# Kernel optimization log

Measured on AMD Instinct MI355X. Metric: run time of the kernel, lower is better.

## Reference

```python
import jax, jax.numpy as jnp
import numpy as np

B, T = 2, 512
E, NH, HD, V, P, L, KER, BLOCK = 768, 12, 64, 256, 4, 4, 16, 512
SCALE = HD ** -0.5


def _ln(x, g, b, eps=1e-5):
    m = jnp.mean(x, -1, keepdims=True)
    v = jnp.mean((x - m) ** 2, -1, keepdims=True)
    return (x - m) * jax.lax.rsqrt(v + eps) * g + b


def _rope_tables(n):
    inv = 1.0 / (10000.0 ** (jnp.arange(0, HD, 2, dtype=jnp.float32) / HD))
    f = jnp.arange(n, dtype=jnp.float32)[:, None] * inv[None, :]
    return jnp.cos(f), jnp.sin(f)


def _rope(x, cos, sin):
    # rotate over last two dims (positions, HD); split-half RoPE as in source
    h = x.shape[-1] // 2
    x1, x2 = x[..., :h], x[..., h:]
    return jnp.concatenate([x1 * cos - x2 * sin, x1 * sin + x2 * cos], axis=-1)


def _patch_attn(x, qkv_w, S):
    # x: [B,T,E]; sliding-window patch attention, step=1
    Bb, Tt, _ = x.shape
    q, k, v = jnp.split(x @ qkv_w, 3, axis=-1)
    heads = lambda t: t.reshape(Bb, Tt, NH, HD).transpose(0, 2, 1, 3)  # [B,NH,T,HD]
    q, k, v = heads(q), heads(k), heads(v)
    cos, sin = _rope_tables(Tt)
    q = _rope(q, cos, sin)
    k = _rope(k, cos, sin)
    # prefix: full causal attention over first S tokens
    sc = jnp.einsum('bnqh,bnkh->bnqk', q[:, :, :S], k[:, :, :S]) * SCALE
    mask = jnp.tril(jnp.ones((S, S), dtype=bool))
    sc = jnp.where(mask, sc, jnp.float32(-jnp.inf))
    out = jnp.einsum('bnqk,bnkh->bnqh', jax.nn.softmax(sc, axis=-1), v[:, :, :S])
    if Tt > S:
        # query t (t>=S) attends keys [t-S+1, t] (mask_sliding is all-ones for step=1)
        idx = jnp.arange(Tt - S)[:, None] + 1 + jnp.arange(S)[None, :]  # [T-S,S]
        kw = k[:, :, idx]  # [B,NH,T-S,S,HD]
        vw = v[:, :, idx]
        qs = q[:, :, S:]   # [B,NH,T-S,HD]
        sw = jnp.einsum('bnth,bntsh->bnts', qs, kw) * SCALE
        ow = jnp.einsum('bnts,bntsh->bnth', jax.nn.softmax(sw, axis=-1), vw)
        out = jnp.concatenate([out, ow], axis=2)
    return out.transpose(0, 2, 1, 3).reshape(Bb, Tt, NH * HD)


def _sa_block(x, ln0g, ln0b, ln1g, ln1b, qkv_w, proj_w, proj_b, w1, b1, w2, b2):
    # x: [B,T,P,V]; full (unmasked) attention over the P prediction slots
    Bb, Tt, Pp, _ = x.shape
    h = _ln(x, ln0g, ln0b)
    q, k, v = jnp.split(h @ qkv_w, 3, axis=-1)
    heads = lambda t: t.reshape(Bb, Tt, Pp, NH, HD).transpose(0, 1, 3, 2, 4)  # [B,T,NH,P,HD]
    q, k, v = heads(q), heads(k), heads(v)
    cos, sin = _rope_tables(Pp)
    q = _rope(q, cos, sin)
    k = _rope(k, cos, sin)
    sc = jnp.einsum('btnph,btnqh->btnpq', q, k) * SCALE
    o = jnp.einsum('btnpq,btnqh->btnph', jax.nn.softmax(sc, axis=-1), v)
    o = o.transpose(0, 1, 3, 2, 4).reshape(Bb, Tt, Pp, NH * HD)
    x = x + (o @ proj_w + proj_b)
    h2 = _ln(x, ln1g, ln1b)
    ff = jax.nn.gelu(h2 @ w1 + b1, approximate=False) @ w2 + b2
    return x + ff


def _forward(tokens, emb, blk_ln0_g, blk_ln0_b, blk_ln1_g, blk_ln1_b, blk_qkv_w,
             blk_ff_w1, blk_ff_b1, blk_ff_w2, blk_ff_b2, fin_ln_g, fin_ln_b,
             head_w, head_b, sa_ln0_g, sa_ln0_b, sa_ln1_g, sa_ln1_b, sa_qkv_w,
             sa_proj_w, sa_proj_b, sa_ff_w1, sa_ff_b1, sa_ff_w2, sa_ff_b2):
    x0 = emb[tokens]  # [B,T,E]
    x = x0
    for i in range(L):
        S = min(KER * 2 ** i, BLOCK)
        h = _ln(x, blk_ln0_g[i], blk_ln0_b[i])
        x = x + _patch_attn(h, blk_qkv_w[i], S)
        h2 = _ln(x, blk_ln1_g[i], blk_ln1_b[i])
        x = x + (jax.nn.gelu(h2 @ blk_ff_w1[i] + blk_ff_b1[i], approximate=False)
                 @ blk_ff_w2[i] + blk_ff_b2[i])
    x = x0 + x  # Golu: x = token_embedding(x); x = x + blocks(x)
    x = _ln(x, fin_ln_g, fin_ln_b)
    logits = (x @ head_w + head_b).reshape(B, T, P, V)
    logits = _sa_block(logits, sa_ln0_g, sa_ln0_b, sa_ln1_g, sa_ln1_b, sa_qkv_w,
                       sa_proj_w, sa_proj_b, sa_ff_w1, sa_ff_b1, sa_ff_w2, sa_ff_b2)
    return logits[:, :, 0, :]  # [B,T,V] (y is None path)


def setup_inputs() -> dict:
    key = jax.random.key(0)
    ks = jax.random.split(key, 12)
    w = lambda k, sh: jax.random.normal(k, sh, dtype=jnp.float32) * 0.02
    return {
        'tokens': jax.random.randint(ks[0], (B, T), 0, V),
        'emb': w(ks[1], (V, E)),
        'blk_ln0_g': jnp.ones((L, E), jnp.float32),
        'blk_ln0_b': jnp.zeros((L, E), jnp.float32),
        'blk_ln1_g': jnp.ones((L, E), jnp.float32),
        'blk_ln1_b': jnp.zeros((L, E), jnp.float32),
        'blk_qkv_w': w(ks[2], (L, E, 3 * E)),
        'blk_ff_w1': w(ks[3], (L, E, 4 * E)),
        'blk_ff_b1': jnp.zeros((L, 4 * E), jnp.float32),
        'blk_ff_w2': w(ks[4], (L, 4 * E, E)),
        'blk_ff_b2': jnp.zeros((L, E), jnp.float32),
        'fin_ln_g': jnp.ones((E,), jnp.float32),
        'fin_ln_b': jnp.zeros((E,), jnp.float32),
        'head_w': w(ks[5], (E, V * P)),
        'head_b': jnp.zeros((V * P,), jnp.float32),
        'sa_ln0_g': jnp.ones((V,), jnp.float32),
        'sa_ln0_b': jnp.zeros((V,), jnp.float32),
        'sa_ln1_g': jnp.ones((V,), jnp.float32),
        'sa_ln1_b': jnp.zeros((V,), jnp.float32),
        'sa_qkv_w': w(ks[6], (V, 3 * E)),
        'sa_proj_w': w(ks[7], (E, V)),
        'sa_proj_b': jnp.zeros((V,), jnp.float32),
        'sa_ff_w1': w(ks[8], (V, 4 * V)),
        'sa_ff_b1': jnp.zeros((4 * V,), jnp.float32),
        'sa_ff_w2': w(ks[9], (4 * V, V)),
        'sa_ff_b2': jnp.zeros((V,), jnp.float32),
    }


def reference(tokens, emb, blk_ln0_g, blk_ln0_b, blk_ln1_g, blk_ln1_b, blk_qkv_w,
              blk_ff_w1, blk_ff_b1, blk_ff_w2, blk_ff_b2, fin_ln_g, fin_ln_b,
              head_w, head_b, sa_ln0_g, sa_ln0_b, sa_ln1_g, sa_ln1_b, sa_qkv_w,
              sa_proj_w, sa_proj_b, sa_ff_w1, sa_ff_b1, sa_ff_w2, sa_ff_b2):
    return _forward(tokens, emb, blk_ln0_g, blk_ln0_b, blk_ln1_g, blk_ln1_b,
                    blk_qkv_w, blk_ff_w1, blk_ff_b1, blk_ff_w2, blk_ff_b2,
                    fin_ln_g, fin_ln_b, head_w, head_b, sa_ln0_g, sa_ln0_b,
                    sa_ln1_g, sa_ln1_b, sa_qkv_w, sa_proj_w, sa_proj_b,
                    sa_ff_w1, sa_ff_b1, sa_ff_w2, sa_ff_b2)
```

## Files before the change

### kernel.cpp

```cpp
#include <hip/hip_runtime.h>
#include <hip/hip_bf16.h>
#include <cstdint>
#include <cstddef>

#define BB    2
#define TSEQ  512
#define EDIM  768
#define NHEAD 12
#define HDIM  64
#define VDIM  256
#define PDIM  4
#define NROW  (BB*TSEQ)
#define NROW2 (BB*TSEQ*PDIM)

typedef __attribute__((ext_vector_type(8))) short short8;
typedef __attribute__((ext_vector_type(4))) float floatx4;

__device__ __forceinline__ float gelu_f(float v){
    return 0.5f * v * (1.0f + erff(v * 0.70710678118654752f));
}
__device__ __forceinline__ float b2f(short s){
    unsigned u = ((unsigned)(unsigned short)s) << 16;
    float f; __builtin_memcpy(&f, &u, 4); return f;
}
__device__ __forceinline__ short f2bs(float v){
    __hip_bfloat16 h = __float2bfloat16(v);
    short s; __builtin_memcpy(&s, &h, 2); return s;
}
__device__ __forceinline__ void gload16(const void* g, void* l){
    __builtin_amdgcn_global_load_lds((const __attribute__((address_space(1))) void*)g,
                                     (__attribute__((address_space(3))) void*)l, 16, 0, 0);
}

struct WD2 { const float* in; __hip_bfloat16* out; int K; int N; int nt; };
struct WDs { WD2 d[17]; };

__global__ __launch_bounds__(256) void wconv_all(WDs a)
{
    int id = blockIdx.x;
    int i = 0;
    while(i < 16 && id >= a.d[i].nt){ id -= a.d[i].nt; i++; }
    WD2 w = a.d[i];
    const int tx = w.N / 64;
    const int n0 = (id % tx) * 64, k0 = (id / tx) * 64;
    __shared__ float t[64][65];
    const int cg = (threadIdx.x & 15) * 4;
    const int rr = threadIdx.x >> 4;
    #pragma unroll
    for(int it = 0; it < 4; it++){
        int r = rr + it*16;
        float4 v = *(const float4*)(w.in + (size_t)(k0 + r) * w.N + n0 + cg);
        t[r][cg+0] = v.x; t[r][cg+1] = v.y; t[r][cg+2] = v.z; t[r][cg+3] = v.w;
    }
    __syncthreads();
    #pragma unroll
    for(int it = 0; it < 4; it++){
        int n = rr + it*16;
        short4 o;
        o.x = f2bs(t[cg+0][n]); o.y = f2bs(t[cg+1][n]);
        o.z = f2bs(t[cg+2][n]); o.w = f2bs(t[cg+3][n]);
        *(short4*)((short*)w.out + (size_t)(n0 + n) * w.K + k0 + cg) = o;
    }
}

template<int ACT, int RESID, int OUTBF16, int ROPESA>
__global__ __launch_bounds__(256) void gemm128(
    const short* __restrict__ A, const short* __restrict__ Bt,
    const float* __restrict__ bias, const float* __restrict__ resid,
    void* __restrict__ Cout, const float* __restrict__ rc, const float* __restrict__ rs,
    int M, int N, int K)
{
    alignas(16) __shared__ short As[128*32];
    alignas(16) __shared__ short Bs[128*32];
    const int tid  = threadIdx.x;
    const int lane = tid & 63;
    const int wave = tid >> 6;
    const int bm = blockIdx.y * 128, bn = blockIdx.x * 128;
    const int wm = (wave >> 1) * 64, wn = (wave & 1) * 64;
    const int quad = lane >> 4, l16 = lane & 15;

    floatx4 acc[4][4];
    #pragma unroll
    for(int i = 0; i < 4; i++)
        #pragma unroll
        for(int j = 0; j < 4; j++)
            acc[i][j] = floatx4{0.f, 0.f, 0.f, 0.f};

    const int r  = tid >> 2;
    const int c8 = (tid & 3) * 8;
    const int ldsoff = (tid & 192) * 16;

    for(int k0 = 0; k0 < K; k0 += 32){
        gload16(A  + (size_t)(bm + r     ) * K + k0 + c8, (char*)As + ldsoff);
        gload16(A  + (size_t)(bm + r + 64) * K + k0 + c8, (char*)As + 4096 + ldsoff);
        gload16(Bt + (size_t)(bn + r     ) * K + k0 + c8, (char*)Bs + ldsoff);
        gload16(Bt + (size_t)(bn + r + 64) * K + k0 + c8, (char*)Bs + 4096 + ldsoff);
        __syncthreads();
        short8 af[4], bfr[4];
        #pragma unroll
        for(int i = 0; i < 4; i++){
            af[i]  = *(const short8*)&As[(wm + i*16 + l16)*32 + quad*8];
            bfr[i] = *(const short8*)&Bs[(wn + i*16 + l16)*32 + quad*8];
        }
        #pragma unroll
        for(int i = 0; i < 4; i++)
            #pragma unroll
            for(int j = 0; j < 4; j++)
                acc[i][j] = __builtin_amdgcn_mfma_f32_16x16x32_bf16(af[i], bfr[j], acc[i][j], 0, 0, 0);
        __syncthreads();
    }

    float* Cf = (float*)Cout;
    __hip_bfloat16* Cb = (__hip_bfloat16*)Cout;

    if(ROPESA){
        const int hb = bn + wn;
        const int region = hb / 768;
        #pragma unroll
        for(int i = 0; i < 4; i++){
            #pragma unroll
            for(int rr = 0; rr < 4; rr++){
                int row = bm + wm + i*16 + quad*4 + rr;
                float a0 = acc[i][0][rr], a1 = acc[i][1][rr];
                float a2 = acc[i][2][rr], a3 = acc[i][3][rr];
                size_t rowb = (size_t)row * N + hb;
                if(region == 2){
                    Cb[rowb + l16]      = __float2bfloat16(a0);
                    Cb[rowb + 16 + l16] = __float2bfloat16(a1);
                    Cb[rowb + 32 + l16] = __float2bfloat16(a2);
                    Cb[rowb + 48 + l16] = __float2bfloat16(a3);
                }else{
                    int p = row & 3;
                    float c0 = rc[p*32 + l16],      s0 = rs[p*32 + l16];
                    float c1 = rc[p*32 + 16 + l16], s1 = rs[p*32 + 16 + l16];
                    Cb[rowb + l16]      = __float2bfloat16(a0*c0 - a2*s0);
                    Cb[rowb + 16 + l16] = __float2bfloat16(a1*c1 - a3*s1);
                    Cb[rowb + 32 + l16] = __float2bfloat16(a0*s0 + a2*c0);
                    Cb[rowb + 48 + l16] = __float2bfloat16(a1*s1 + a3*c1);
                }
            }
        }
        return;
    }

    #pragma unroll
    for(int i = 0; i < 4; i++){
        int row0 = bm + wm + i*16 + quad*4;
        #pragma unroll
        for(int j = 0; j < 4; j++){
            int col = bn + wn + j*16 + l16;
            float bv = bias ? bias[col] : 0.f;
            #pragma unroll
            for(int rr = 0; rr < 4; rr++){
                float v = acc[i][j][rr] + bv;
                if(ACT) v = gelu_f(v);
                if(RESID) v += resid[(size_t)(row0 + rr) * N + col];
                if(OUTBF16) Cb[(size_t)(row0 + rr) * N + col] = __float2bfloat16(v);
                else        Cf[(size_t)(row0 + rr) * N + col] = v;
            }
        }
    }
}

template<int EPI>
__global__ __launch_bounds__(256) void gemm64x128(
    const short* __restrict__ A, const short* __restrict__ Bt,
    const float* __restrict__ bias, __hip_bfloat16* __restrict__ Cout,
    __hip_bfloat16* __restrict__ qrb, __hip_bfloat16* __restrict__ krb,
    __hip_bfloat16* __restrict__ vvb,
    const float* __restrict__ rc, const float* __restrict__ rs,
    int M, int N, int K)
{
    alignas(16) __shared__ short As[64*32];
    alignas(16) __shared__ short Bs[128*32];
    const int tid  = threadIdx.x;
    const int lane = tid & 63;
    const int wave = tid >> 6;
    const int bm = blockIdx.y * 64, bn = blockIdx.x * 128;
    const int wm = (wave >> 1) * 32, wn = (wave & 1) * 64;
    const int quad = lane >> 4, l16 = lane & 15;

    floatx4 acc[2][4];
    #pragma unroll
    for(int i = 0; i < 2; i++)
        #pragma unroll
        for(int j = 0; j < 4; j++)
            acc[i][j] = floatx4{0.f, 0.f, 0.f, 0.f};

    const int r  = tid >> 2;
    const int c8 = (tid & 3) * 8;
    const int ldsoff = (tid & 192) * 16;

    for(int k0 = 0; k0 < K; k0 += 32){
        gload16(A  + (size_t)(bm + r     ) * K + k0 + c8, (char*)As + ldsoff);
        gload16(Bt + (size_t)(bn + r     ) * K + k0 + c8, (char*)Bs + ldsoff);
        gload16(Bt + (size_t)(bn + r + 64) * K + k0 + c8, (char*)Bs + 4096 + ldsoff);
        __syncthreads();
        short8 af[2], bfr[4];
        #pragma unroll
        for(int i = 0; i < 2; i++)
            af[i]  = *(const short8*)&As[(wm + i*16 + l16)*32 + quad*8];
        #pragma unroll
        for(int j = 0; j < 4; j++)
            bfr[j] = *(const short8*)&Bs[(wn + j*16 + l16)*32 + quad*8];
        #pragma unroll
        for(int i = 0; i < 2; i++)
            #pragma unroll
            for(int j = 0; j < 4; j++)
                acc[i][j] = __builtin_amdgcn_mfma_f32_16x16x32_bf16(af[i], bfr[j], acc[i][j], 0, 0, 0);
        __syncthreads();
    }

    if(EPI == 2){
        const int hb = bn + wn;
        const int region = hb / 768;
        const int h = (hb % 768) >> 6;
        #pragma unroll
        for(int i = 0; i < 2; i++){
            #pragma unroll
            for(int rr = 0; rr < 4; rr++){
                int row = bm + wm + i*16 + quad*4 + rr;
                int t = row & (TSEQ-1), b = row >> 9;
                float a0 = acc[i][0][rr], a1 = acc[i][1][rr];
                float a2 = acc[i][2][rr], a3 = acc[i][3][rr];
                size_t dbase = ((size_t)(b*NHEAD + h)*TSEQ + t)*HDIM;
                if(region == 2){
                    vvb[dbase + l16]      = __float2bfloat16(a0);
                    vvb[dbase + 16 + l16] = __float2bfloat16(a1);
                    vvb[dbase + 32 + l16] = __float2bfloat16(a2);
                    vvb[dbase + 48 + l16] = __float2bfloat16(a3);
                }else{
                    float c0 = rc[t*32 + l16],      s0 = rs[t*32 + l16];
                    float c1 = rc[t*32 + 16 + l16], s1 = rs[t*32 + 16 + l16];
                    __hip_bfloat16* dst = (region == 0) ? qrb : krb;
                    dst[dbase + l16]      = __float2bfloat16(a0*c0 - a2*s0);
                    dst[dbase + 16 + l16] = __float2bfloat16(a1*c1 - a3*s1);
                    dst[dbase + 32 + l16] = __float2bfloat16(a0*s0 + a2*c0);
                    dst[dbase + 48 + l16] = __float2bfloat16(a1*s1 + a3*c1);
                }
            }
        }
        return;
    }

    #pragma unroll
    for(int i = 0; i < 2; i++){
        int row0 = bm + wm + i*16 + quad*4;
        #pragma unroll
        for(int j = 0; j < 4; j++){
            int col = bn + wn + j*16 + l16;
            float bv = bias ? bias[col] : 0.f;
            #pragma unroll
            for(int rr = 0; rr < 4; rr++){
                float v = acc[i][j][rr] + bv;
                if(EPI == 1) v = gelu_f(v);
                Cout[(size_t)(row0 + rr) * N + col] = __float2bfloat16(v);
            }
        }
    }
}

template<int RESID, int OUTC>
__global__ __launch_bounds__(256) void gemm64t(
    const short* __restrict__ A, const short* __restrict__ Bt,
    const float* __restrict__ bias, const float* __restrict__ resid,
    float* __restrict__ Cf, float* __restrict__ outp, int M, int N, int K)
{
    alignas(16) __shared__ short As[64*32];
    alignas(16) __shared__ short Bs[64*32];
    const int tid  = threadIdx.x;
    const int lane = tid & 63;
    const int wave = tid >> 6;
    const int bm = blockIdx.y * 64, bn = blockIdx.x * 64;
    const int wm = (wave >> 1) * 32, wn = (wave & 1) * 32;
    const int quad = lane >> 4, l16 = lane & 15;

    floatx4 acc[2][2];
    #pragma unroll
    for(int i = 0; i < 2; i++)
        #pragma unroll
        for(int j = 0; j < 2; j++)
            acc[i][j] = floatx4{0.f, 0.f, 0.f, 0.f};

    const int r  = tid >> 2;
    const int c8 = (tid & 3) * 8;
    const int ldsoff = (tid & 192) * 16;

    for(int k0 = 0; k0 < K; k0 += 32){
        gload16(A  + (size_t)(bm + r) * K + k0 + c8, (char*)As + ldsoff);
        gload16(Bt + (size_t)(bn + r) * K + k0 + c8, (char*)Bs + ldsoff);
        __syncthreads();
        short8 af[2], bfr[2];
        #pragma unroll
        for(int i = 0; i < 2; i++){
            af[i]  = *(const short8*)&As[(wm + i*16 + l16)*32 + quad*8];
            bfr[i] = *(const short8*)&Bs[(wn + i*16 + l16)*32 + quad*8];
        }
        #pragma unroll
        for(int i = 0; i < 2; i++)
            #pragma unroll
            for(int j = 0; j < 2; j++)
                acc[i][j] = __builtin_amdgcn_mfma_f32_16x16x32_bf16(af[i], bfr[j], acc[i][j], 0, 0, 0);
        __syncthreads();
    }

    #pragma unroll
    for(int i = 0; i < 2; i++){
        int row0 = bm + wm + i*16 + quad*4;
        #pragma unroll
        for(int j = 0; j < 2; j++){
            int col = bn + wn + j*16 + l16;
            float bv = bias ? bias[col] : 0.f;
            #pragma unroll
            for(int rr = 0; rr < 4; rr++){
                int row = row0 + rr;
                float v = acc[i][j][rr] + bv;
                if(RESID) v += resid[(size_t)row * N + col];
                Cf[(size_t)row * N + col] = v;
                if(OUTC && (row & 3) == 0)
                    outp[(size_t)(row >> 2) * N + col] = v;
            }
        }
    }
}

__global__ __launch_bounds__(256) void ln_kernel(
    const float* __restrict__ in, const float* __restrict__ in2,
    const float* __restrict__ g, const float* __restrict__ bta,
    __hip_bfloat16* __restrict__ out, int D)
{
    const int row = blockIdx.x;
    const float* xr  = in + (size_t)row * D;
    const float* x2r = in2 ? in2 + (size_t)row * D : nullptr;
    const int tid = threadIdx.x;
    const int nper = D / 256;
    float vals[3];
    float sum = 0.f, sq = 0.f;
    for(int i = 0; i < nper; i++){
        int d = tid + i*256;
        float v = xr[d];
        if(x2r) v += x2r[d];
        vals[i] = v; sum += v; sq += v*v;
    }
    #pragma unroll
    for(int off = 32; off > 0; off >>= 1){
        sum += __shfl_xor(sum, off, 64);
        sq  += __shfl_xor(sq,  off, 64);
    }
    __shared__ float ssum[4], ssq[4];
    __shared__ float smean, srstd;
    int wid = tid >> 6;
    if((tid & 63) == 0){ ssum[wid] = sum; ssq[wid] = sq; }
    __syncthreads();
    if(tid == 0){
        float S = 0.f, Q = 0.f;
        for(int w = 0; w < 4; w++){ S += ssum[w]; Q += ssq[w]; }
        float m = S / D;
        float var = Q / D - m*m;
        smean = m;
        srstd = rsqrtf(fmaxf(var, 0.f) + 1e-5f);
    }
    __syncthreads();
    float m = smean, rs2 = srstd;
    for(int i = 0; i < nper; i++){
        int d = tid + i*256;
        out[(size_t)row*D + d] = __float2bfloat16((vals[i] - m) * rs2 * g[d] + bta[d]);
    }
}

__global__ __launch_bounds__(192) void embed_kernel(
    const int* __restrict__ tokens, const float* __restrict__ emb,
    float* __restrict__ x0, float* __restrict__ x)
{
    const int row = blockIdx.x;
    const int tok = tokens[row];
    const float4* src = (const float4*)(emb + (size_t)tok * EDIM);
    float4* d0 = (float4*)(x0 + (size_t)row * EDIM);
    float4* d1 = (float4*)(x  + (size_t)row * EDIM);
    for(int i = threadIdx.x; i < EDIM/4; i += blockDim.x){
        float4 v = src[i]; d0[i] = v; d1[i] = v;
    }
}

__global__ __launch_bounds__(256) void rope_kernel(float* __restrict__ rc, float* __restrict__ rs)
{
    int i = blockIdx.x * 256 + threadIdx.x;
    int pos = i >> 5, d = i & 31;
    float inv = powf(10000.0f, -(float)(2*d) / 64.0f);
    float f = (float)pos * inv;
    rc[i] = cosf(f);
    rs[i] = sinf(f);
}

template<int S>
__global__ __launch_bounds__(256) void patch_attn2(
    const __hip_bfloat16* __restrict__ qr, const __hip_bfloat16* __restrict__ kr,
    const __hip_bfloat16* __restrict__ vv, float* __restrict__ x)
{
    constexpr int W = S + 3;
    alignas(16) __shared__ short Ks[W*64];
    alignas(16) __shared__ short Vs[W*64];
    __shared__ float qlds[4*64];
    __shared__ float pb[4*128];

    const int t0 = blockIdx.x * 4;
    const int h = blockIdx.y, b = blockIdx.z;
    const int tid = threadIdx.x;
    const int wv = tid >> 6, lane = tid & 63;
    const size_t headbase = ((size_t)(b*NHEAD + h)) * TSEQ;

    const int c = tid & 7;
    for(int r = tid >> 3; r < W; r += 32){
        int g = t0 - S + 1 + r;
        int gc = g < 0 ? 0 : g;
        int sc = (c ^ (r & 7)) * 8;
        *(short8*)&Ks[r*64 + sc] = *(const short8*)((const short*)kr + (headbase + gc)*64 + c*8);
        *(short8*)&Vs[r*64 + sc] = *(const short8*)((const short*)vv + (headbase + gc)*64 + c*8);
    }
    qlds[wv*64 + lane] = __bfloat162float(qr[(headbase + t0 + wv)*64 + lane]);
    __syncthreads();

    const int t = t0 + wv;
    const int r0 = (S >= 64) ? (wv + lane) : ((lane < S) ? (wv + lane) : 0);
    const int r1 = wv + lane + 64;
    float a0 = 0.f, a1 = 0.f;
    #pragma unroll
    for(int ch = 0; ch < 8; ch++){
        float4 qa = *(const float4*)&qlds[wv*64 + ch*8];
        float4 qb = *(const float4*)&qlds[wv*64 + ch*8 + 4];
        short8 k0 = *(const short8*)&Ks[r0*64 + ((ch ^ (r0 & 7))*8)];
        a0 += qa.x*b2f(k0[0]) + qa.y*b2f(k0[1]) + qa.z*b2f(k0[2]) + qa.w*b2f(k0[3])
            + qb.x*b2f(k0[4]) + qb.y*b2f(k0[5]) + qb.z*b2f(k0[6]) + qb.w*b2f(k0[7]);
        if(S == 128){
            short8 k1 = *(const short8*)&Ks[r1*64 + ((ch ^ (r1 & 7))*8)];
            a1 += qa.x*b2f(k1[0]) + qa.y*b2f(k1[1]) + qa.z*b2f(k1[2]) + qa.w*b2f(k1[3])
                + qb.x*b2f(k1[4]) + qb.y*b2f(k1[5]) + qb.z*b2f(k1[6]) + qb.w*b2f(k1[7]);
        }
    }
    const int key0 = t - S + 1 + lane;
    const bool v0 = (lane < S) && (key0 >= 0);
    const bool v1 = (S == 128) && (key0 + 64 >= 0);
    float s0 = v0 ? a0 * 0.125f : -1e30f;
    float s1 = v1 ? a1 * 0.125f : -1e30f;
    float mx = fmaxf(s0, s1);
    #pragma unroll
    for(int off = 32; off > 0; off >>= 1) mx = fmaxf(mx, __shfl_xor(mx, off, 64));
    float p0 = v0 ? expf(s0 - mx) : 0.f;
    float p1 = v1 ? expf(s1 - mx) : 0.f;
    float sm = p0 + p1;
    #pragma unroll
    for(int off = 32; off > 0; off >>= 1) sm += __shfl_xor(sm, off, 64);
    const float inv = 1.f / sm;
    pb[wv*128 + lane] = p0 * inv;
    if(S == 128) pb[wv*128 + lane + 64] = p1 * inv;
    __syncthreads();

    const int d = lane;
    const int coff = d >> 3, dlo = d & 7;
    float o = 0.f;
    #pragma unroll 8
    for(int j = 0; j < S; j++){
        int r = wv + j;
        float p = pb[wv*128 + j];
        o += p * b2f(Vs[r*64 + ((coff ^ (r & 7))*8) + dlo]);
    }
    x[((size_t)(b*TSEQ) + t) * EDIM + h*HDIM + d] += o;
}

__global__ __launch_bounds__(256) void sa_attn(
    const __hip_bfloat16* __restrict__ qkv2, __hip_bfloat16* __restrict__ o)
{
    const int t = blockIdx.x, h = blockIdx.y, b = blockIdx.z;
    const int p = threadIdx.x >> 6, lane = threadIdx.x & 63;
    const int row0 = (b*TSEQ + t) * PDIM;
    const short* base = (const short*)qkv2 + (size_t)row0 * (3*EDIM);
    const int d = lane;
    float q = b2f(base[(size_t)p*(3*EDIM) + h*HDIM + d]);
    float sc[4];
    #pragma unroll
    for(int j = 0; j < 4; j++){
        float kj = b2f(base[(size_t)j*(3*EDIM) + EDIM + h*HDIM + d]);
        float v = q * kj;
        #pragma unroll
        for(int off = 32; off > 0; off >>= 1) v += __shfl_xor(v, off, 64);
        sc[j] = v * 0.125f;
    }
    float m = fmaxf(fmaxf(sc[0], sc[1]), fmaxf(sc[2], sc[3]));
    float e0 = expf(sc[0]-m), e1 = expf(sc[1]-m), e2 = expf(sc[2]-m), e3 = expf(sc[3]-m);
    float idn = 1.f / (e0 + e1 + e2 + e3);
    float ov = (e0 * b2f(base[0*(3*EDIM) + 2*EDIM + h*HDIM + d])
              + e1 * b2f(base[1*(3*EDIM) + 2*EDIM + h*HDIM + d])
              + e2 * b2f(base[2*(3*EDIM) + 2*EDIM + h*HDIM + d])
              + e3 * b2f(base[3*(3*EDIM) + 2*EDIM + h*HDIM + d])) * idn;
    o[(size_t)(row0 + p) * EDIM + h*HDIM + d] = __float2bfloat16(ov);
}

extern "C" void kernel_launch(void* const* d_in, const int* in_sizes, int n_in,
                              void* d_out, int out_size, void* d_ws, size_t ws_size,
                              hipStream_t stream)
{
    const int*   tokens    = (const int*)  d_in[0];
    const float* emb       = (const float*)d_in[1];
    const float* bl0g      = (const float*)d_in[2];
    const float* bl0b      = (const float*)d_in[3];
    const float* bl1g      = (const float*)d_in[4];
    const float* bl1b      = (const float*)d_in[5];
    const float* qkv_w     = (const float*)d_in[6];
    const float* ff_w1     = (const float*)d_in[7];
    const float* ff_b1     = (const float*)d_in[8];
    const float* ff_w2     = (const float*)d_in[9];
    const float* ff_b2     = (const float*)d_in[10];
    const float* fin_g     = (const float*)d_in[11];
    const float* fin_b     = (const float*)d_in[12];
    const float* head_w    = (const float*)d_in[13];
    const float* head_b    = (const float*)d_in[14];
    const float* sa_ln0_g  = (const float*)d_in[15];
    const float* sa_ln0_b  = (const float*)d_in[16];
    const float* sa_ln1_g  = (const float*)d_in[17];
    const float* sa_ln1_b  = (const float*)d_in[18];
    const float* sa_qkv_w  = (const float*)d_in[19];
    const float* sa_proj_w = (const float*)d_in[20];
    const float* sa_proj_b = (const float*)d_in[21];
    const float* sa_ff_w1  = (const float*)d_in[22];
    const float* sa_ff_b1  = (const float*)d_in[23];
    const float* sa_ff_w2  = (const float*)d_in[24];
    const float* sa_ff_b2  = (const float*)d_in[25];
    float* out = (float*)d_out;

    char* p = (char*)d_ws;
    auto alloc = [&](size_t bytes){ char* q = p; p += (bytes + 255) & ~(size_t)255; return q; };

    float* logits = (float*)alloc((size_t)NROW2*VDIM*4);
    float* ropec  = (float*)alloc(512*32*4);
    float* ropes  = (float*)alloc(512*32*4);
    __hip_bfloat16* wqkvT[4]; for(int i=0;i<4;i++) wqkvT[i] = (__hip_bfloat16*)alloc((size_t)768*2304*2);
    __hip_bfloat16* wff1T[4]; for(int i=0;i<4;i++) wff1T[i] = (__hip_bfloat16*)alloc((size_t)768*3072*2);
    __hip_bfloat16* wff2T[4]; for(int i=0;i<4;i++) wff2T[i] = (__hip_bfloat16*)alloc((size_t)3072*768*2);
    __hip_bfloat16* wheadT   = (__hip_bfloat16*)alloc((size_t)768*1024*2);
    __hip_bfloat16* wsaqkvT  = (__hip_bfloat16*)alloc((size_t)256*2304*2);
    __hip_bfloat16* wsaprojT = (__hip_bfloat16*)alloc((size_t)768*256*2);
    __hip_bfloat16* wsaff1T  = (__hip_bfloat16*)alloc((size_t)256*1024*2);
    __hip_bfloat16* wsaff2T  = (__hip_bfloat16*)alloc((size_t)1024*256*2);
    char* U = p;
    float* x0           = (float*)(U);
    float* x            = (float*)(U + 3145728);
    __hip_bfloat16* h   = (__hip_bfloat16*)(U + 6291456);
    __hip_bfloat16* ff1 = (__hip_bfloat16*)(U + 7864320);
    __hip_bfloat16* qrb = (__hip_bfloat16*)(U + 14155776);
    __hip_bfloat16* krb = (__hip_bfloat16*)(U + 15728640);
    __hip_bfloat16* vvb = (__hip_bfloat16*)(U + 17301504);
    __hip_bfloat16* h2    = (__hip_bfloat16*)(U);
    __hip_bfloat16* qkv2  = (__hip_bfloat16*)(U + 2097152);
    __hip_bfloat16* sa_o  = (__hip_bfloat16*)(U + 20971520);
    __hip_bfloat16* sa_f1 = (__hip_bfloat16*)(U + 27262976);

    embed_kernel<<<NROW, 192, 0, stream>>>(tokens, emb, x0, x);
    rope_kernel<<<64, 256, 0, stream>>>(ropec, ropes);
    {
        WDs wds; int tot = 0, n = 0;
        auto add = [&](const float* in, __hip_bfloat16* o2, int K, int N){
            wds.d[n++] = WD2{in, o2, K, N, (N/64)*(K/64)};
            tot += (N/64)*(K/64);
        };
        for(int i=0;i<4;i++){
            add(qkv_w + (size_t)i*768*2304, wqkvT[i], 768, 2304);
            add(ff_w1 + (size_t)i*768*3072, wff1T[i], 768, 3072);
            add(ff_w2 + (size_t)i*3072*768, wff2T[i], 3072, 768);
        }
        add(head_w,    wheadT,   768, 1024);
        add(sa_qkv_w,  wsaqkvT,  256, 2304);
        add(sa_proj_w, wsaprojT, 768, 256);
        add(sa_ff_w1,  wsaff1T,  256, 1024);
        add(sa_ff_w2,  wsaff2T, 1024, 256);
        wconv_all<<<tot, 256, 0, stream>>>(wds);
    }

    for(int i = 0; i < 4; i++){
        ln_kernel<<<NROW, 256, 0, stream>>>(x, nullptr, bl0g + i*EDIM, bl0b + i*EDIM, h, EDIM);
        gemm64x128<2><<<dim3(18, 16), 256, 0, stream>>>(
            (const short*)h, (const short*)wqkvT[i], nullptr, nullptr,
            qrb, krb, vvb, ropec, ropes, NROW, 3*EDIM, EDIM);
        dim3 agrid(TSEQ/4, NHEAD, BB);
        if(i == 0)      patch_attn2<16><<<agrid, 256, 0, stream>>>(qrb, krb, vvb, x);
        else if(i == 1) patch_attn2<32><<<agrid, 256, 0, stream>>>(qrb, krb, vvb, x);
        else if(i == 2) patch_attn2<64><<<agrid, 256, 0, stream>>>(qrb, krb, vvb, x);
        else            patch_attn2<128><<<agrid, 256, 0, stream>>>(qrb, krb, vvb, x);
        ln_kernel<<<NROW, 256, 0, stream>>>(x, nullptr, bl1g + i*EDIM, bl1b + i*EDIM, h, EDIM);
        gemm64x128<1><<<dim3(24, 16), 256, 0, stream>>>(
            (const short*)h, (const short*)wff1T[i], ff_b1 + (size_t)i*4*EDIM, ff1,
            nullptr, nullptr, nullptr, nullptr, nullptr, NROW, 4*EDIM, EDIM);
        gemm64t<1,0><<<dim3(12, 16), 256, 0, stream>>>(
            (const short*)ff1, (const short*)wff2T[i], ff_b2 + (size_t)i*EDIM, x, x, nullptr,
            NROW, EDIM, 4*EDIM);
    }

    ln_kernel<<<NROW, 256, 0, stream>>>(x, x0, fin_g, fin_b, h, EDIM);
    gemm64t<0,0><<<dim3(16, 16), 256, 0, stream>>>(
        (const short*)h, (const short*)wheadT, head_b, nullptr, logits, nullptr,
        NROW, PDIM*VDIM, EDIM);

    ln_kernel<<<NROW2, 256, 0, stream>>>(logits, nullptr, sa_ln0_g, sa_ln0_b, h2, VDIM);
    gemm128<0,0,1,1><<<dim3(18, 32), 256, 0, stream>>>(
        (const short*)h2, (const short*)wsaqkvT, nullptr, nullptr, qkv2,
        ropec, ropes, NROW2, 3*EDIM, VDIM);
    sa_attn<<<dim3(TSEQ, NHEAD, BB), 256, 0, stream>>>(qkv2, sa_o);
    gemm64t<1,0><<<dim3(4, 64), 256, 0, stream>>>(
        (const short*)sa_o, (const short*)wsaprojT, sa_proj_b, logits, logits, nullptr,
        NROW2, VDIM, EDIM);
    ln_kernel<<<NROW2, 256, 0, stream>>>(logits, nullptr, sa_ln1_g, sa_ln1_b, h2, VDIM);
    gemm128<1,0,1,0><<<dim3(8, 32), 256, 0, stream>>>(
        (const short*)h2, (const short*)wsaff1T, sa_ff_b1, nullptr, sa_f1,
        nullptr, nullptr, NROW2, 4*VDIM, VDIM);
    gemm64t<1,1><<<dim3(4, 64), 256, 0, stream>>>(
        (const short*)sa_f1, (const short*)wsaff2T, sa_ff_b2, logits, logits, out,
        NROW2, VDIM, 4*VDIM);
}
```

Before: 704.1 us.

## Double-buffer LDS tiles in GEMM kernels and widen weight-convert stores

```diff
diff --git a/kernel.cpp b/kernel.cpp
--- a/kernel.cpp
+++ b/kernel.cpp
@@ -16,6 +16,8 @@
 typedef __attribute__((ext_vector_type(8))) short short8;
 typedef __attribute__((ext_vector_type(4))) float floatx4;
 
+#define PIPE_BARRIER asm volatile("s_waitcnt vmcnt(0)\n\ts_barrier" ::: "memory")
+
 __device__ __forceinline__ float gelu_f(float v){
     return 0.5f * v * (1.0f + erff(v * 0.70710678118654752f));
 }
@@ -44,22 +46,28 @@
     const int tx = w.N / 64;
     const int n0 = (id % tx) * 64, k0 = (id / tx) * 64;
     __shared__ float t[64][65];
-    const int cg = (threadIdx.x & 15) * 4;
-    const int rr = threadIdx.x >> 4;
-    #pragma unroll
-    for(int it = 0; it < 4; it++){
-        int r = rr + it*16;
-        float4 v = *(const float4*)(w.in + (size_t)(k0 + r) * w.N + n0 + cg);
-        t[r][cg+0] = v.x; t[r][cg+1] = v.y; t[r][cg+2] = v.z; t[r][cg+3] = v.w;
+    {
+        const int cg = (threadIdx.x & 15) * 4;
+        const int rr = threadIdx.x >> 4;
+        #pragma unroll
+        for(int it = 0; it < 4; it++){
+            int r = rr + it*16;
+            float4 v = *(const float4*)(w.in + (size_t)(k0 + r) * w.N + n0 + cg);
+            t[r][cg+0] = v.x; t[r][cg+1] = v.y; t[r][cg+2] = v.z; t[r][cg+3] = v.w;
+        }
     }
     __syncthreads();
-    #pragma unroll
-    for(int it = 0; it < 4; it++){
-        int n = rr + it*16;
-        short4 o;
-        o.x = f2bs(t[cg+0][n]); o.y = f2bs(t[cg+1][n]);
-        o.z = f2bs(t[cg+2][n]); o.w = f2bs(t[cg+3][n]);
-        *(short4*)((short*)w.out + (size_t)(n0 + n) * w.K + k0 + cg) = o;
+    {
+        const int cg8 = (threadIdx.x & 7) * 8;
+        const int nn  = threadIdx.x >> 3;
+        #pragma unroll
+        for(int pass = 0; pass < 2; pass++){
+            int n = nn + pass*32;
+            short8 o;
+            #pragma unroll
+            for(int j = 0; j < 8; j++) o[j] = f2bs(t[cg8 + j][n]);
+            *(short8*)((short*)w.out + (size_t)(n0 + n) * w.K + k0 + cg8) = o;
+        }
     }
 }
 
@@ -70,8 +78,8 @@
     void* __restrict__ Cout, const float* __restrict__ rc, const float* __restrict__ rs,
     int M, int N, int K)
 {
-    alignas(16) __shared__ short As[128*32];
-    alignas(16) __shared__ short Bs[128*32];
+    alignas(16) __shared__ short As[2*128*32];
+    alignas(16) __shared__ short Bs[2*128*32];
     const int tid  = threadIdx.x;
     const int lane = tid & 63;
     const int wave = tid >> 6;
@@ -90,24 +98,33 @@
     const int c8 = (tid & 3) * 8;
     const int ldsoff = (tid & 192) * 16;
 
-    for(int k0 = 0; k0 < K; k0 += 32){
-        gload16(A  + (size_t)(bm + r     ) * K + k0 + c8, (char*)As + ldsoff);
-        gload16(A  + (size_t)(bm + r + 64) * K + k0 + c8, (char*)As + 4096 + ldsoff);
-        gload16(Bt + (size_t)(bn + r     ) * K + k0 + c8, (char*)Bs + ldsoff);
-        gload16(Bt + (size_t)(bn + r + 64) * K + k0 + c8, (char*)Bs + 4096 + ldsoff);
-        __syncthreads();
+    auto issue = [&](int k0, int cur){
+        char* ab = (char*)As + cur*8192 + ldsoff;
+        char* bb = (char*)Bs + cur*8192 + ldsoff;
+        gload16(A  + (size_t)(bm + r     ) * K + k0 + c8, ab);
+        gload16(A  + (size_t)(bm + r + 64) * K + k0 + c8, ab + 4096);
+        gload16(Bt + (size_t)(bn + r     ) * K + k0 + c8, bb);
+        gload16(Bt + (size_t)(bn + r + 64) * K + k0 + c8, bb + 4096);
+    };
+
+    const int niter = K >> 5;
+    issue(0, 0);
+    for(int it = 0; it < niter; it++){
+        PIPE_BARRIER;
+        if(it + 1 < niter) issue((it + 1) << 5, (it + 1) & 1);
+        const short* Ab = As + (it & 1) * 4096;
+        const short* Bb = Bs + (it & 1) * 4096;
         short8 af[4], bfr[4];
         #pragma unroll
         for(int i = 0; i < 4; i++){
-            af[i]  = *(const short8*)&As[(wm + i*16 + l16)*32 + quad*8];
-            bfr[i] = *(const short8*)&Bs[(wn + i*16 + l16)*32 + quad*8];
+            af[i]  = *(const short8*)&Ab[(wm + i*16 + l16)*32 + quad*8];
+            bfr[i] = *(const short8*)&Bb[(wn + i*16 + l16)*32 + quad*8];
         }
         #pragma unroll
         for(int i = 0; i < 4; i++)
             #pragma unroll
             for(int j = 0; j < 4; j++)
                 acc[i][j] = __builtin_amdgcn_mfma_f32_16x16x32_bf16(af[i], bfr[j], acc[i][j], 0, 0, 0);
-        __syncthreads();
     }
 
     float* Cf = (float*)Cout;
@@ -171,8 +188,8 @@
     const float* __restrict__ rc, const float* __restrict__ rs,
     int M, int N, int K)
 {
-    alignas(16) __shared__ short As[64*32];
-    alignas(16) __shared__ short Bs[128*32];
+    alignas(16) __shared__ short As[2*64*32];
+    alignas(16) __shared__ short Bs[2*128*32];
     const int tid  = threadIdx.x;
     const int lane = tid & 63;
     const int wave = tid >> 6;
@@ -191,24 +208,33 @@
     const int c8 = (tid & 3) * 8;
     const int ldsoff = (tid & 192) * 16;
 
-    for(int k0 = 0; k0 < K; k0 += 32){
-        gload16(A  + (size_t)(bm + r     ) * K + k0 + c8, (char*)As + ldsoff);
-        gload16(Bt + (size_t)(bn + r     ) * K + k0 + c8, (char*)Bs + ldsoff);
-        gload16(Bt + (size_t)(bn + r + 64) * K + k0 + c8, (char*)Bs + 4096 + ldsoff);
-        __syncthreads();
+    auto issue = [&](int k0, int cur){
+        char* ab = (char*)As + cur*4096 + ldsoff;
+        char* bb = (char*)Bs + cur*8192 + ldsoff;
+        gload16(A  + (size_t)(bm + r     ) * K + k0 + c8, ab);
+        gload16(Bt + (size_t)(bn + r     ) * K + k0 + c8, bb);
+        gload16(Bt + (size_t)(bn + r + 64) * K + k0 + c8, bb + 4096);
+    };
+
+    const int niter = K >> 5;
+    issue(0, 0);
+    for(int it = 0; it < niter; it++){
+        PIPE_BARRIER;
+        if(it + 1 < niter) issue((it + 1) << 5, (it + 1) & 1);
+        const short* Ab = As + (it & 1) * 2048;
+        const short* Bb = Bs + (it & 1) * 4096;
         short8 af[2], bfr[4];
         #pragma unroll
         for(int i = 0; i < 2; i++)
-            af[i]  = *(const short8*)&As[(wm + i*16 + l16)*32 + quad*8];
+            af[i]  = *(const short8*)&Ab[(wm + i*16 + l16)*32 + quad*8];
         #pragma unroll
         for(int j = 0; j < 4; j++)
-            bfr[j] = *(const short8*)&Bs[(wn + j*16 + l16)*32 + quad*8];
+            bfr[j] = *(const short8*)&Bb[(wn + j*16 + l16)*32 + quad*8];
         #pragma unroll
         for(int i = 0; i < 2; i++)
             #pragma unroll
             for(int j = 0; j < 4; j++)
                 acc[i][j] = __builtin_amdgcn_mfma_f32_16x16x32_bf16(af[i], bfr[j], acc[i][j], 0, 0, 0);
-        __syncthreads();
     }
 
     if(EPI == 2){
@@ -266,8 +292,8 @@
     const float* __restrict__ bias, const float* __restrict__ resid,
     float* __restrict__ Cf, float* __restrict__ outp, int M, int N, int K)
 {
-    alignas(16) __shared__ short As[64*32];
-    alignas(16) __shared__ short Bs[64*32];
+    alignas(16) __shared__ short As[2*64*32];
+    alignas(16) __shared__ short Bs[2*64*32];
     const int tid  = threadIdx.x;
     const int lane = tid & 63;
     const int wave = tid >> 6;
@@ -286,22 +312,31 @@
     const int c8 = (tid & 3) * 8;
     const int ldsoff = (tid & 192) * 16;
 
-    for(int k0 = 0; k0 < K; k0 += 32){
-        gload16(A  + (size_t)(bm + r) * K + k0 + c8, (char*)As + ldsoff);
-        gload16(Bt + (size_t)(bn + r) * K + k0 + c8, (char*)Bs + ldsoff);
-        __syncthreads();
+    auto issue = [&](int k0, int cur){
+        char* ab = (char*)As + cur*4096 + ldsoff;
+        char* bb = (char*)Bs + cur*4096 + ldsoff;
+        gload16(A  + (size_t)(bm + r) * K + k0 + c8, ab);
+        gload16(Bt + (size_t)(bn + r) * K + k0 + c8, bb);
+    };
+
+    const int niter = K >> 5;
+    issue(0, 0);
+    for(int it = 0; it < niter; it++){
+        PIPE_BARRIER;
+        if(it + 1 < niter) issue((it + 1) << 5, (it + 1) & 1);
+        const short* Ab = As + (it & 1) * 2048;
+        const short* Bb = Bs + (it & 1) * 2048;
         short8 af[2], bfr[2];
         #pragma unroll
         for(int i = 0; i < 2; i++){
-            af[i]  = *(const short8*)&As[(wm + i*16 + l16)*32 + quad*8];
-            bfr[i] = *(const short8*)&Bs[(wn + i*16 + l16)*32 + quad*8];
+            af[i]  = *(const short8*)&Ab[(wm + i*16 + l16)*32 + quad*8];
+            bfr[i] = *(const short8*)&Bb[(wn + i*16 + l16)*32 + quad*8];
         }
         #pragma unroll
         for(int i = 0; i < 2; i++)
             #pragma unroll
             for(int j = 0; j < 2; j++)
                 acc[i][j] = __builtin_amdgcn_mfma_f32_16x16x32_bf16(af[i], bfr[j], acc[i][j], 0, 0, 0);
-        __syncthreads();
     }
 
     #pragma unroll
```

Result: no change. 699.0 us (-0.7%).
